# Kernel optimization log

Hardware: AMD Instinct MI355X
Metric: run time of the kernel (lower is better)

Reference implementation:

```python
import jax, jax.numpy as jnp
import numpy as np

B, D, U, BR, IU, HID = 1024, 2048, 4096, 4, 3072, 32


def setup_inputs() -> dict:
    key = jax.random.key(0)
    ks = jax.random.split(key, 12)
    inputs = jax.random.normal(ks[0], (B, D), dtype=jnp.float32)
    # dendritic kernel / bias / delay (glorot-ish scale)
    w = jax.random.normal(ks[1], (D, U, BR), dtype=jnp.float32) * 0.02
    b = jax.random.normal(ks[2], (U, BR), dtype=jnp.float32) * 0.01
    delay = jax.random.normal(ks[3], (D, U, BR), dtype=jnp.float32) * 0.5
    # branch gating dense (softmax applied in reference)
    Wg = jax.random.normal(ks[4], (D, BR), dtype=jnp.float32) * 0.02
    bg = jnp.zeros((BR,), dtype=jnp.float32)
    # DynamicConnectivity attention net: Dense(32, relu) -> Dense(U, sigmoid)
    W1 = jax.random.normal(ks[5], (U, HID), dtype=jnp.float32) * 0.02
    b1 = jnp.zeros((HID,), dtype=jnp.float32)
    W2 = jax.random.normal(ks[6], (HID, U), dtype=jnp.float32) * 0.02
    b2 = jnp.zeros((U,), dtype=jnp.float32)
    # non-trainable state
    neuron_mask = jnp.concatenate([jnp.ones((IU,), jnp.float32), jnp.zeros((U - IU,), jnp.float32)])
    neuron_activation_avg = jax.random.uniform(ks[7], (U,), dtype=jnp.float32) * 0.1
    return {"inputs": inputs, "w": w, "b": b, "delay": delay, "Wg": Wg, "bg": bg,
            "W1": W1, "b1": b1, "W2": W2, "b2": b2,
            "neuron_mask": neuron_mask, "neuron_activation_avg": neuron_activation_avg}


def reference(inputs, w, b, delay, Wg, bg, W1, b1, W2, b2, neuron_mask, neuron_activation_avg):
    # sigmoid-gated weights, 3-way tensordot -> [B, U, BR]
    w_mod = w * jax.nn.sigmoid(delay)
    branch_outputs = jnp.einsum('bd,duk->buk', inputs, w_mod) + b
    # per-branch softmax gating from the input, soft combine over branches
    gating = jax.nn.softmax(inputs @ Wg + bg, axis=-1)            # [B, BR]
    z_combined = jnp.einsum('buk,bk->bu', branch_outputs, gating)  # [B, U]
    # dynamic connectivity from neuron activation EMA state: [1, U]
    h = jax.nn.relu(neuron_activation_avg[None, :] @ W1 + b1)
    connectivity = jax.nn.sigmoid(h @ W2 + b2)                     # [1, U]
    z_modulated = z_combined * connectivity * neuron_mask[None, :]
    a = jax.nn.relu(z_modulated)
    return a
```

## Files before the change

kernel.cpp:

```cpp
#include <hip/hip_runtime.h>
#include <cstdint>
#include <cstddef>

typedef __bf16 bf16;
typedef __bf16 bf16x4 __attribute__((ext_vector_type(4)));
typedef __bf16 bf16x8 __attribute__((ext_vector_type(8)));
typedef float f32x4 __attribute__((ext_vector_type(4)));

#define B_SZ 1024
#define D_SZ 2048
#define U_SZ 4096
#define BR_SZ 4
#define N_SZ (U_SZ * BR_SZ)

#define WS_WT 0
#define WS_A (64u * 1024u * 1024u)
#define WS_GAT (WS_A + 4u * 1024u * 1024u)
#define WS_CONN (WS_GAT + 16384u)
#define WS_H (WS_CONN + 16384u)

__device__ __forceinline__ float sigmoidf_(float x) { return 1.f / (1.f + __expf(-x)); }

__global__ void k0_convert(const float* __restrict__ in, bf16* __restrict__ a,
                           float* __restrict__ wsh) {
  int idx = blockIdx.x * 256 + threadIdx.x;
  if (idx < 32) wsh[idx] = 0.f;
  float4 v = ((const float4*)in)[idx];
  bf16x4 o;
  o[0] = (bf16)v.x; o[1] = (bf16)v.y; o[2] = (bf16)v.z; o[3] = (bf16)v.w;
  ((bf16x4*)a)[idx] = o;
}

__global__ void k1_gating(const float* __restrict__ in, const float* __restrict__ Wg,
                          const float* __restrict__ bg, float* __restrict__ gat) {
  int row = blockIdx.x, tid = threadIdx.x;
  float a0 = 0, a1 = 0, a2 = 0, a3 = 0;
  const float* ir = in + row * D_SZ;
  for (int d = tid; d < D_SZ; d += 256) {
    float x = ir[d];
    float4 wg = ((const float4*)Wg)[d];
    a0 += x * wg.x; a1 += x * wg.y; a2 += x * wg.z; a3 += x * wg.w;
  }
#pragma unroll
  for (int off = 32; off; off >>= 1) {
    a0 += __shfl_down(a0, off); a1 += __shfl_down(a1, off);
    a2 += __shfl_down(a2, off); a3 += __shfl_down(a3, off);
  }
  __shared__ float red[4][4];
  int wv = tid >> 6, ln = tid & 63;
  if (ln == 0) { red[wv][0] = a0; red[wv][1] = a1; red[wv][2] = a2; red[wv][3] = a3; }
  __syncthreads();
  if (tid == 0) {
    float s0 = red[0][0] + red[1][0] + red[2][0] + red[3][0] + bg[0];
    float s1 = red[0][1] + red[1][1] + red[2][1] + red[3][1] + bg[1];
    float s2 = red[0][2] + red[1][2] + red[2][2] + red[3][2] + bg[2];
    float s3 = red[0][3] + red[1][3] + red[2][3] + red[3][3] + bg[3];
    float m = fmaxf(fmaxf(s0, s1), fmaxf(s2, s3));
    float e0 = __expf(s0 - m), e1 = __expf(s1 - m), e2 = __expf(s2 - m), e3 = __expf(s3 - m);
    float inv = 1.f / (e0 + e1 + e2 + e3);
    ((float4*)gat)[row] = make_float4(e0 * inv, e1 * inv, e2 * inv, e3 * inv);
  }
}

__global__ void k2a_h(const float* __restrict__ avg, const float* __restrict__ W1,
                      float* __restrict__ wsh) {
  int t = threadIdx.x;
  int h = t & 31, seg = t >> 5;
  int u0 = blockIdx.x * 64 + seg * 8;
  float p = 0.f;
#pragma unroll
  for (int j = 0; j < 8; j++) {
    int u = u0 + j;
    p += avg[u] * W1[u * 32 + h];
  }
  __shared__ float red[8][32];
  red[seg][h] = p;
  __syncthreads();
  if (t < 32) {
    float s = 0.f;
#pragma unroll
    for (int sg = 0; sg < 8; sg++) s += red[sg][t];
    atomicAdd(&wsh[t], s);
  }
}

__global__ void k2b_conn(const float* __restrict__ wsh, const float* __restrict__ b1,
                         const float* __restrict__ W2, const float* __restrict__ b2,
                         const float* __restrict__ mask, float* __restrict__ conn) {
  int u = blockIdx.x * 256 + threadIdx.x;
  __shared__ float hv[32];
  if (threadIdx.x < 32) hv[threadIdx.x] = fmaxf(wsh[threadIdx.x] + b1[threadIdx.x], 0.f);
  __syncthreads();
  float s = b2[u];
#pragma unroll
  for (int h = 0; h < 32; h++) s += hv[h] * W2[h * U_SZ + u];
  conn[u] = sigmoidf_(s) * mask[u];
}

#define TP 72
__global__ void k3_wmod_t(const float* __restrict__ w, const float* __restrict__ delay,
                          bf16* __restrict__ wt) {
  __shared__ bf16 t[64 * TP];
  int tid = threadIdx.x;
  int n0 = blockIdx.x * 64, d0 = blockIdx.y * 64;
#pragma unroll
  for (int i = 0; i < 4; i++) {
    int flat = i * 256 + tid;
    int d = flat >> 4, n4 = flat & 15;
    int gi = (d0 + d) * N_SZ + n0 + n4 * 4;
    float4 wv = *(const float4*)(w + gi);
    float4 dv = *(const float4*)(delay + gi);
    t[(n4 * 4 + 0) * TP + d] = (bf16)(wv.x * sigmoidf_(dv.x));
    t[(n4 * 4 + 1) * TP + d] = (bf16)(wv.y * sigmoidf_(dv.y));
    t[(n4 * 4 + 2) * TP + d] = (bf16)(wv.z * sigmoidf_(dv.z));
    t[(n4 * 4 + 3) * TP + d] = (bf16)(wv.w * sigmoidf_(dv.w));
  }
  __syncthreads();
#pragma unroll
  for (int p = 0; p < 2; p++) {
    int flat = p * 256 + tid;
    int n = flat >> 3, d8 = flat & 7;
    bf16x8 v = *(const bf16x8*)&t[n * TP + d8 * 8];
    *(bf16x8*)(wt + (size_t)(n0 + n) * D_SZ + d0 + d8 * 8) = v;
  }
}

__global__ __launch_bounds__(256, 2) void k4_gemm(
    const bf16* __restrict__ A, const bf16* __restrict__ Bt,
    const float* __restrict__ gating, const float* __restrict__ bias,
    const float* __restrict__ conn, float* __restrict__ out) {
  __shared__ bf16 Al[128 * 64];
  __shared__ bf16 Bl[128 * 64];
  __shared__ float gat[128 * 4];
  int tid = threadIdx.x;
  int lane = tid & 63, wave = tid >> 6;
  int bid = blockIdx.x;
  int mt = bid & 7, nt = bid >> 3;
  int m0 = mt * 128, n0 = nt * 128;
  int wm = (wave & 1) * 64, wn = (wave >> 1) * 64;
  int quad = lane >> 4, row16 = lane & 15;

  f32x4 acc[4][4];
  const f32x4 z4 = {0.f, 0.f, 0.f, 0.f};
#pragma unroll
  for (int i = 0; i < 4; i++)
#pragma unroll
    for (int j = 0; j < 4; j++) acc[i][j] = z4;

  if (tid < 128) *(float4*)&gat[tid * 4] = *(const float4*)&gating[(m0 + tid) * 4];

  int srow = lane >> 3, scol = (lane & 7) * 8;
  for (int kt = 0; kt < 32; kt++) {
    int k0 = kt * 64;
#pragma unroll
    for (int c = 0; c < 4; c++) {
      int rb = wave * 32 + c * 8;
      const bf16* ga = A + (size_t)(m0 + rb + srow) * D_SZ + k0 + scol;
      __builtin_amdgcn_global_load_lds(
          (const __attribute__((address_space(1))) void*)ga,
          (__attribute__((address_space(3))) void*)(Al + rb * 64), 16, 0, 0);
      const bf16* gb = Bt + (size_t)(n0 + rb + srow) * D_SZ + k0 + scol;
      __builtin_amdgcn_global_load_lds(
          (const __attribute__((address_space(1))) void*)gb,
          (__attribute__((address_space(3))) void*)(Bl + rb * 64), 16, 0, 0);
    }
    __syncthreads();
#pragma unroll
    for (int kk = 0; kk < 64; kk += 32) {
      bf16x8 af[4], bfr[4];
#pragma unroll
      for (int i = 0; i < 4; i++)
        af[i] = *(const bf16x8*)&Al[(wm + i * 16 + row16) * 64 + kk + quad * 8];
#pragma unroll
      for (int j = 0; j < 4; j++)
        bfr[j] = *(const bf16x8*)&Bl[(wn + j * 16 + row16) * 64 + kk + quad * 8];
#pragma unroll
      for (int i = 0; i < 4; i++)
#pragma unroll
        for (int j = 0; j < 4; j++)
          acc[i][j] = __builtin_amdgcn_mfma_f32_16x16x32_bf16(af[i], bfr[j], acc[i][j], 0, 0, 0);
    }
    __syncthreads();
  }

  int k = lane & 3;
#pragma unroll
  for (int j = 0; j < 4; j++) {
    int n_l = wn + j * 16 + row16;
    int n_g = n0 + n_l;
    int u = n_g >> 2;
    float bv = bias[n_g];
    float cv = conn[u];
#pragma unroll
    for (int i = 0; i < 4; i++) {
#pragma unroll
      for (int r = 0; r < 4; r++) {
        int r_l = wm + i * 16 + quad * 4 + r;
        float g = gat[r_l * 4 + k];
        float v = (acc[i][j][r] + bv) * g;
        v += __shfl_xor(v, 1);
        v += __shfl_xor(v, 2);
        if (k == 0) out[(size_t)(m0 + r_l) * U_SZ + u] = fmaxf(v * cv, 0.f);
      }
    }
  }
}

extern "C" void kernel_launch(void* const* d_in, const int* in_sizes, int n_in,
                              void* d_out, int out_size, void* d_ws, size_t ws_size,
                              hipStream_t stream) {
  const float* inputs = (const float*)d_in[0];
  const float* w = (const float*)d_in[1];
  const float* bb = (const float*)d_in[2];
  const float* delay = (const float*)d_in[3];
  const float* Wg = (const float*)d_in[4];
  const float* bg = (const float*)d_in[5];
  const float* W1 = (const float*)d_in[6];
  const float* b1 = (const float*)d_in[7];
  const float* W2 = (const float*)d_in[8];
  const float* b2 = (const float*)d_in[9];
  const float* mask = (const float*)d_in[10];
  const float* avg = (const float*)d_in[11];
  float* out = (float*)d_out;
  char* ws = (char*)d_ws;
  bf16* wt = (bf16*)(ws + WS_WT);
  bf16* wa = (bf16*)(ws + WS_A);
  float* gat = (float*)(ws + WS_GAT);
  float* cn = (float*)(ws + WS_CONN);
  float* wsh = (float*)(ws + WS_H);

  hipLaunchKernelGGL(k0_convert, dim3((B_SZ * D_SZ / 4) / 256), dim3(256), 0, stream, inputs, wa, wsh);
  hipLaunchKernelGGL(k1_gating, dim3(B_SZ), dim3(256), 0, stream, inputs, Wg, bg, gat);
  hipLaunchKernelGGL(k2a_h, dim3(U_SZ / 64), dim3(256), 0, stream, avg, W1, wsh);
  hipLaunchKernelGGL(k2b_conn, dim3(U_SZ / 256), dim3(256), 0, stream, wsh, b1, W2, b2, mask, cn);
  hipLaunchKernelGGL(k3_wmod_t, dim3(N_SZ / 64, D_SZ / 64), dim3(256), 0, stream, w, delay, wt);
  hipLaunchKernelGGL(k4_gemm, dim3((B_SZ / 128) * (N_SZ / 128)), dim3(256), 0, stream, wa, wt, gat, bb, cn, out);
}
```

Before: 421.5 us.

## Fuse prep kernels, swizzle GEMM LDS, remap blocks per XCD, pipeline weight transpose

Merges the input bf16 conversion and the gating softmax into one pass over each input row, and folds the connectivity computation into the GEMM prologue, which removes two kernel launches and one intermediate buffer. The GEMM gets an XOR-swizzled LDS layout to cut bank conflicts, plus a block-to-tile mapping that groups N tiles per XCD for better L2 reuse. The weight-modulation transpose kernel now walks 256 rows of D per block with double-buffered packed shared memory, overlapping loads with stores. The cost is that each GEMM block redoes a small 32x32 connectivity matvec, and the kernel code grows more complex.

```diff
diff --git a/kernel.cpp b/kernel.cpp
--- a/kernel.cpp
+++ b/kernel.cpp
@@ -16,30 +16,36 @@
 #define WS_WT 0
 #define WS_A (64u * 1024u * 1024u)
 #define WS_GAT (WS_A + 4u * 1024u * 1024u)
-#define WS_CONN (WS_GAT + 16384u)
-#define WS_H (WS_CONN + 16384u)
+#define WS_H (WS_GAT + 16384u)
 
 __device__ __forceinline__ float sigmoidf_(float x) { return 1.f / (1.f + __expf(-x)); }
 
-__global__ void k0_convert(const float* __restrict__ in, bf16* __restrict__ a,
-                           float* __restrict__ wsh) {
-  int idx = blockIdx.x * 256 + threadIdx.x;
-  if (idx < 32) wsh[idx] = 0.f;
-  float4 v = ((const float4*)in)[idx];
-  bf16x4 o;
-  o[0] = (bf16)v.x; o[1] = (bf16)v.y; o[2] = (bf16)v.z; o[3] = (bf16)v.w;
-  ((bf16x4*)a)[idx] = o;
-}
-
-__global__ void k1_gating(const float* __restrict__ in, const float* __restrict__ Wg,
-                          const float* __restrict__ bg, float* __restrict__ gat) {
+__device__ __forceinline__ uint32_t pack2_(float lo, float hi) {
+  union { bf16 h[2]; uint32_t u; } cv;
+  cv.h[0] = (bf16)lo; cv.h[1] = (bf16)hi;
+  return cv.u;
+}
+
+__global__ void k01_prep(const float* __restrict__ in, bf16* __restrict__ wa,
+                         const float* __restrict__ Wg, const float* __restrict__ bg,
+                         float* __restrict__ gat, float* __restrict__ wsh) {
   int row = blockIdx.x, tid = threadIdx.x;
+  if (row == 0 && tid < 32) wsh[tid] = 0.f;
+  const float* ir = in + (size_t)row * D_SZ;
   float a0 = 0, a1 = 0, a2 = 0, a3 = 0;
-  const float* ir = in + row * D_SZ;
-  for (int d = tid; d < D_SZ; d += 256) {
-    float x = ir[d];
-    float4 wg = ((const float4*)Wg)[d];
-    a0 += x * wg.x; a1 += x * wg.y; a2 += x * wg.z; a3 += x * wg.w;
+#pragma unroll
+  for (int c = 0; c < 2; c++) {
+    int d = c * 1024 + tid * 4;
+    float4 x = *(const float4*)(ir + d);
+    bf16x4 o;
+    o[0] = (bf16)x.x; o[1] = (bf16)x.y; o[2] = (bf16)x.z; o[3] = (bf16)x.w;
+    *(bf16x4*)(wa + (size_t)row * D_SZ + d) = o;
+    const float xs[4] = {x.x, x.y, x.z, x.w};
+#pragma unroll
+    for (int j = 0; j < 4; j++) {
+      float4 wg = ((const float4*)Wg)[d + j];
+      a0 += xs[j] * wg.x; a1 += xs[j] * wg.y; a2 += xs[j] * wg.z; a3 += xs[j] * wg.w;
+    }
   }
 #pragma unroll
   for (int off = 32; off; off >>= 1) {
@@ -84,61 +90,86 @@
   }
 }
 
-__global__ void k2b_conn(const float* __restrict__ wsh, const float* __restrict__ b1,
-                         const float* __restrict__ W2, const float* __restrict__ b2,
-                         const float* __restrict__ mask, float* __restrict__ conn) {
-  int u = blockIdx.x * 256 + threadIdx.x;
-  __shared__ float hv[32];
-  if (threadIdx.x < 32) hv[threadIdx.x] = fmaxf(wsh[threadIdx.x] + b1[threadIdx.x], 0.f);
-  __syncthreads();
-  float s = b2[u];
-#pragma unroll
-  for (int h = 0; h < 32; h++) s += hv[h] * W2[h * U_SZ + u];
-  conn[u] = sigmoidf_(s) * mask[u];
-}
-
-#define TP 72
-__global__ void k3_wmod_t(const float* __restrict__ w, const float* __restrict__ delay,
-                          bf16* __restrict__ wt) {
-  __shared__ bf16 t[64 * TP];
+#define K3P 33
+__global__ __launch_bounds__(256) void k3_wmod_t(const float* __restrict__ w,
+                                                 const float* __restrict__ delay,
+                                                 bf16* __restrict__ wt) {
+  __shared__ uint32_t buf[2][64 * K3P];
   int tid = threadIdx.x;
-  int n0 = blockIdx.x * 64, d0 = blockIdx.y * 64;
-#pragma unroll
-  for (int i = 0; i < 4; i++) {
-    int flat = i * 256 + tid;
-    int d = flat >> 4, n4 = flat & 15;
-    int gi = (d0 + d) * N_SZ + n0 + n4 * 4;
-    float4 wv = *(const float4*)(w + gi);
-    float4 dv = *(const float4*)(delay + gi);
-    t[(n4 * 4 + 0) * TP + d] = (bf16)(wv.x * sigmoidf_(dv.x));
-    t[(n4 * 4 + 1) * TP + d] = (bf16)(wv.y * sigmoidf_(dv.y));
-    t[(n4 * 4 + 2) * TP + d] = (bf16)(wv.z * sigmoidf_(dv.z));
-    t[(n4 * 4 + 3) * TP + d] = (bf16)(wv.w * sigmoidf_(dv.w));
-  }
-  __syncthreads();
-#pragma unroll
-  for (int p = 0; p < 2; p++) {
-    int flat = p * 256 + tid;
-    int n = flat >> 3, d8 = flat & 7;
-    bf16x8 v = *(const bf16x8*)&t[n * TP + d8 * 8];
-    *(bf16x8*)(wt + (size_t)(n0 + n) * D_SZ + d0 + d8 * 8) = v;
+  int n0 = blockIdx.x * 64;
+  int d0 = blockIdx.y * 256;
+  int d2 = tid >> 4, n4 = tid & 15;
+  int p2n = tid >> 3, p2o = tid & 7;
+
+  float4 rw[4], rd[4];
+
+#define K3_LOAD(t)                                                         \
+  {                                                                        \
+    _Pragma("unroll") for (int pass = 0; pass < 2; pass++) {               \
+      int d = d0 + (t) * 64 + pass * 32 + d2 * 2;                          \
+      size_t g = (size_t)d * N_SZ + n0 + n4 * 4;                           \
+      rw[pass * 2 + 0] = *(const float4*)(w + g);                          \
+      rw[pass * 2 + 1] = *(const float4*)(w + g + N_SZ);                   \
+      rd[pass * 2 + 0] = *(const float4*)(delay + g);                      \
+      rd[pass * 2 + 1] = *(const float4*)(delay + g + N_SZ);               \
+    }                                                                      \
+  }
+#define K3_WRITE(bsel)                                                     \
+  {                                                                        \
+    _Pragma("unroll") for (int pass = 0; pass < 2; pass++) {               \
+      const float* fw0 = (const float*)&rw[pass * 2 + 0];                  \
+      const float* fw1 = (const float*)&rw[pass * 2 + 1];                  \
+      const float* fd0 = (const float*)&rd[pass * 2 + 0];                  \
+      const float* fd1 = (const float*)&rd[pass * 2 + 1];                  \
+      _Pragma("unroll") for (int j = 0; j < 4; j++) {                      \
+        float lo = fw0[j] * sigmoidf_(fd0[j]);                             \
+        float hi = fw1[j] * sigmoidf_(fd1[j]);                             \
+        buf[bsel][(n4 * 4 + j) * K3P + pass * 16 + d2] = pack2_(lo, hi);   \
+      }                                                                    \
+    }                                                                      \
+  }
+#define K3_STORE(t, bsel)                                                  \
+  {                                                                        \
+    int dt = d0 + (t) * 64;                                                \
+    _Pragma("unroll") for (int pass = 0; pass < 2; pass++) {               \
+      int n = pass * 32 + p2n;                                             \
+      const uint32_t* r = &buf[bsel][n * K3P + p2o * 4];                   \
+      uint4 v;                                                             \
+      v.x = r[0]; v.y = r[1]; v.z = r[2]; v.w = r[3];                      \
+      *(uint4*)(wt + (size_t)(n0 + n) * D_SZ + dt + p2o * 8) = v;          \
+    }                                                                      \
+  }
+
+  K3_LOAD(0);
+  K3_WRITE(0);
+#pragma unroll
+  for (int t = 0; t < 4; t++) {
+    __syncthreads();
+    if (t < 3) K3_LOAD(t + 1);
+    K3_STORE(t, (t & 1));
+    if (t < 3) K3_WRITE(((t + 1) & 1));
   }
 }
 
 __global__ __launch_bounds__(256, 2) void k4_gemm(
     const bf16* __restrict__ A, const bf16* __restrict__ Bt,
     const float* __restrict__ gating, const float* __restrict__ bias,
-    const float* __restrict__ conn, float* __restrict__ out) {
+    const float* __restrict__ wsh, const float* __restrict__ b1,
+    const float* __restrict__ W2, const float* __restrict__ b2,
+    const float* __restrict__ mask, float* __restrict__ out) {
   __shared__ bf16 Al[128 * 64];
   __shared__ bf16 Bl[128 * 64];
   __shared__ float gat[128 * 4];
+  __shared__ float conn_l[32];
   int tid = threadIdx.x;
   int lane = tid & 63, wave = tid >> 6;
   int bid = blockIdx.x;
-  int mt = bid & 7, nt = bid >> 3;
+  int xcd = bid & 7, p = bid >> 3;
+  int mt = p & 7, nt = (xcd << 4) | (p >> 3);
   int m0 = mt * 128, n0 = nt * 128;
   int wm = (wave & 1) * 64, wn = (wave >> 1) * 64;
   int quad = lane >> 4, row16 = lane & 15;
+  int r7 = row16 & 7;
 
   f32x4 acc[4][4];
   const f32x4 z4 = {0.f, 0.f, 0.f, 0.f};
@@ -148,8 +179,16 @@
     for (int j = 0; j < 4; j++) acc[i][j] = z4;
 
   if (tid < 128) *(float4*)&gat[tid * 4] = *(const float4*)&gating[(m0 + tid) * 4];
-
-  int srow = lane >> 3, scol = (lane & 7) * 8;
+  if (tid < 32) {
+    int u = (n0 >> 2) + tid;
+    float s = b2[u];
+#pragma unroll
+    for (int h = 0; h < 32; h++) s += fmaxf(wsh[h] + b1[h], 0.f) * W2[h * U_SZ + u];
+    conn_l[tid] = sigmoidf_(s) * mask[u];
+  }
+
+  int srow = lane >> 3;
+  int scol = ((lane & 7) ^ srow) * 8;
   for (int kt = 0; kt < 32; kt++) {
     int k0 = kt * 64;
 #pragma unroll
@@ -167,13 +206,14 @@
     __syncthreads();
 #pragma unroll
     for (int kk = 0; kk < 64; kk += 32) {
+      int csw = (((kk >> 3) + quad) ^ r7) * 8;
       bf16x8 af[4], bfr[4];
 #pragma unroll
       for (int i = 0; i < 4; i++)
-        af[i] = *(const bf16x8*)&Al[(wm + i * 16 + row16) * 64 + kk + quad * 8];
+        af[i] = *(const bf16x8*)&Al[(wm + i * 16 + row16) * 64 + csw];
 #pragma unroll
       for (int j = 0; j < 4; j++)
-        bfr[j] = *(const bf16x8*)&Bl[(wn + j * 16 + row16) * 64 + kk + quad * 8];
+        bfr[j] = *(const bf16x8*)&Bl[(wn + j * 16 + row16) * 64 + csw];
 #pragma unroll
       for (int i = 0; i < 4; i++)
 #pragma unroll
@@ -190,7 +230,7 @@
     int n_g = n0 + n_l;
     int u = n_g >> 2;
     float bv = bias[n_g];
-    float cv = conn[u];
+    float cv = conn_l[n_l >> 2];
 #pragma unroll
     for (int i = 0; i < 4; i++) {
 #pragma unroll
@@ -226,13 +266,10 @@
   bf16* wt = (bf16*)(ws + WS_WT);
   bf16* wa = (bf16*)(ws + WS_A);
   float* gat = (float*)(ws + WS_GAT);
-  float* cn = (float*)(ws + WS_CONN);
   float* wsh = (float*)(ws + WS_H);
 
-  hipLaunchKernelGGL(k0_convert, dim3((B_SZ * D_SZ / 4) / 256), dim3(256), 0, stream, inputs, wa, wsh);
-  hipLaunchKernelGGL(k1_gating, dim3(B_SZ), dim3(256), 0, stream, inputs, Wg, bg, gat);
+  hipLaunchKernelGGL(k01_prep, dim3(B_SZ), dim3(256), 0, stream, inputs, wa, Wg, bg, gat, wsh);
   hipLaunchKernelGGL(k2a_h, dim3(U_SZ / 64), dim3(256), 0, stream, avg, W1, wsh);
-  hipLaunchKernelGGL(k2b_conn, dim3(U_SZ / 256), dim3(256), 0, stream, wsh, b1, W2, b2, mask, cn);
-  hipLaunchKernelGGL(k3_wmod_t, dim3(N_SZ / 64, D_SZ / 64), dim3(256), 0, stream, w, delay, wt);
-  hipLaunchKernelGGL(k4_gemm, dim3((B_SZ / 128) * (N_SZ / 128)), dim3(256), 0, stream, wa, wt, gat, bb, cn, out);
-}
+  hipLaunchKernelGGL(k3_wmod_t, dim3(N_SZ / 64, D_SZ / 256), dim3(256), 0, stream, w, delay, wt);
+  hipLaunchKernelGGL(k4_gemm, dim3((B_SZ / 128) * (N_SZ / 128)), dim3(256), 0, stream, wa, wt, gat, bb, wsh, b1, W2, b2, mask, out);
+}
```

Result: faster. 389.6 us (-7.6%).
